# Performance work log

Hardware: AMD Instinct MI355X
Metric: run time of the kernel (lower is better)

The kernel has to match this reference:

```python
import jax, jax.numpy as jnp
import numpy as np

B, N = 16, 4096          # batch, path tokens
D, H = 512, 2048         # dim, 4*dim
NG, NP, NF = 4, 4, 2     # expert counts
GIN, PIN, NC = 4096, 1024, 4
EPS = 1e-5


def _ln_norm(x):
    # LayerNorm normalization (biased var, eps=1e-5), affine applied by caller
    m = jnp.mean(x, axis=-1, keepdims=True)
    v = jnp.var(x, axis=-1, keepdims=True)
    return (x - m) * jax.lax.rsqrt(v + EPS)


def _expert_mlp(xn, ln_g, ln_b, W1, b1, W2, b2):
    # xn: [B,D] or [E,B,D] (pre-normalized); per-expert affine + MLP (GELU exact)
    h = xn * ln_g[:, None, :] + ln_b[:, None, :]            # [E,B,D]
    h = jax.nn.gelu(jnp.einsum('ebd,edh->ebh', h, W1) + b1[:, None, :], approximate=False)
    return jnp.einsum('ebh,ehd->ebd', h, W2) + b2[:, None, :]


def setup_inputs() -> dict:
    key = jax.random.key(0)
    ks = iter(jax.random.split(key, 64))
    nrm = lambda shape, s=0.02: jax.random.normal(next(ks), shape, jnp.float32) * s
    return {
        'F_gene': jax.random.normal(next(ks), (B, GIN), jnp.float32),
        'F_path': jax.random.normal(next(ks), (B, N, PIN), jnp.float32),
        'gene_ln_g': jnp.ones((GIN,)), 'gene_ln_b': jnp.zeros((GIN,)),
        'gene_W': nrm((GIN, D)), 'gene_b': jnp.zeros((D,)),
        'path_ln_g': jnp.ones((PIN,)), 'path_ln_b': jnp.zeros((PIN,)),
        'path_W': nrm((PIN, D)), 'path_b': jnp.zeros((D,)),
        'g_ln_g': jnp.ones((NG, D)), 'g_ln_b': jnp.zeros((NG, D)),
        'g_W1': nrm((NG, D, H)), 'g_b1': jnp.zeros((NG, H)),
        'g_W2': nrm((NG, H, D)), 'g_b2': jnp.zeros((NG, D)),
        'p_q': jax.random.normal(next(ks), (NP, D), jnp.float32),
        'p_ln_g': jnp.ones((NP, D)), 'p_ln_b': jnp.zeros((NP, D)),
        'p_W1': nrm((NP, D, H)), 'p_b1': jnp.zeros((NP, H)),
        'p_W2': nrm((NP, H, D)), 'p_b2': jnp.zeros((NP, D)),
        'f_ln_g': jnp.ones((NF, D)), 'f_ln_b': jnp.zeros((NF, D)),
        'f_W1': nrm((NF, D, H)), 'f_b1': jnp.zeros((NF, H)),
        'f_W2': nrm((NF, H, D)), 'f_b2': jnp.zeros((NF, D)),
        'gg_ln_g': jnp.ones((D,)), 'gg_ln_b': jnp.zeros((D,)),
        'gg_W': nrm((D, NG)), 'gg_b': jnp.zeros((NG,)),
        'pg_ln_g': jnp.ones((D,)), 'pg_ln_b': jnp.zeros((D,)),
        'pg_W': nrm((D, NP)), 'pg_b': jnp.zeros((NP,)),
        'fg_ln_g': jnp.ones((2 * D,)), 'fg_ln_b': jnp.zeros((2 * D,)),
        'fg_W': nrm((2 * D, NF)), 'fg_b': jnp.zeros((NF,)),
        'fin_ln_g': jnp.ones((2 * D,)), 'fin_ln_b': jnp.zeros((2 * D,)),
        'fin_W': nrm((2 * D, D)), 'fin_b': jnp.zeros((D,)),
        'cls_W': nrm((D, NC)), 'cls_b': jnp.zeros((NC,)),
    }


def _forward(F_gene, F_path, gene_ln_g, gene_ln_b, gene_W, gene_b,
             path_ln_g, path_ln_b, path_W, path_b,
             g_ln_g, g_ln_b, g_W1, g_b1, g_W2, g_b2,
             p_q, p_ln_g, p_ln_b, p_W1, p_b1, p_W2, p_b2,
             f_ln_g, f_ln_b, f_W1, f_b1, f_W2, f_b2,
             gg_ln_g, gg_ln_b, gg_W, gg_b,
             pg_ln_g, pg_ln_b, pg_W, pg_b,
             fg_ln_g, fg_ln_b, fg_W, fg_b,
             fin_ln_g, fin_ln_b, fin_W, fin_b, cls_W, cls_b):
    # input projections
    Xg = (_ln_norm(F_gene) * gene_ln_g + gene_ln_b) @ gene_W + gene_b      # [B,D]
    Xp = (_ln_norm(F_path) * path_ln_g + path_ln_b) @ path_W + path_b      # [B,N,D]

    # gene experts: shared gated mixture of MLPs
    wg = jax.nn.softmax((_ln_norm(Xg) * gg_ln_g + gg_ln_b) @ gg_W + gg_b, axis=-1)  # [B,NG]
    g_stack = _expert_mlp(_ln_norm(Xg), g_ln_g, g_ln_b, g_W1, g_b1, g_W2, g_b2)     # [NG,B,D]
    FGIMF = jnp.einsum('be,ebd->bd', wg, g_stack)

    # path experts: per-expert attention pooling over N tokens, then MLP
    Xp_mean = jnp.mean(Xp, axis=1)                                                  # [B,D]
    wp = jax.nn.softmax((_ln_norm(Xp_mean) * pg_ln_g + pg_ln_b) @ pg_W + pg_b, axis=-1)
    attn = jax.nn.softmax(jnp.einsum('bnd,ed->ebn', Xp, p_q), axis=-1)              # [NP,B,N]
    pooled = jnp.einsum('ebn,bnd->ebd', attn, Xp)                                   # [NP,B,D]
    p_stack = _expert_mlp(_ln_norm(pooled), p_ln_g, p_ln_b, p_W1, p_b1, p_W2, p_b2)
    FPIMF = jnp.einsum('be,ebd->bd', wp, p_stack)

    # fusion experts
    fused = jnp.concatenate([FGIMF, FPIMF], axis=-1)                                # [B,2D]
    wf = jax.nn.softmax((_ln_norm(fused) * fg_ln_g + fg_ln_b) @ fg_W + fg_b, axis=-1)
    fused_in = (_ln_norm(fused) * fin_ln_g + fin_ln_b) @ fin_W + fin_b              # [B,D]
    f_stack = _expert_mlp(_ln_norm(fused_in), f_ln_g, f_ln_b, f_W1, f_b1, f_W2, f_b2)
    FIMMF = jnp.einsum('be,ebd->bd', wf, f_stack)

    logits = FIMMF @ cls_W + cls_b
    hazards = jax.nn.sigmoid(logits)
    S = jnp.cumprod(1.0 - hazards, axis=1)
    return hazards, S


def reference(F_gene, F_path, gene_ln_g, gene_ln_b, gene_W, gene_b,
              path_ln_g, path_ln_b, path_W, path_b,
              g_ln_g, g_ln_b, g_W1, g_b1, g_W2, g_b2,
              p_q, p_ln_g, p_ln_b, p_W1, p_b1, p_W2, p_b2,
              f_ln_g, f_ln_b, f_W1, f_b1, f_W2, f_b2,
              gg_ln_g, gg_ln_b, gg_W, gg_b,
              pg_ln_g, pg_ln_b, pg_W, pg_b,
              fg_ln_g, fg_ln_b, fg_W, fg_b,
              fin_ln_g, fin_ln_b, fin_W, fin_b, cls_W, cls_b):
    return _forward(F_gene, F_path, gene_ln_g, gene_ln_b, gene_W, gene_b,
                    path_ln_g, path_ln_b, path_W, path_b,
                    g_ln_g, g_ln_b, g_W1, g_b1, g_W2, g_b2,
                    p_q, p_ln_g, p_ln_b, p_W1, p_b1, p_W2, p_b2,
                    f_ln_g, f_ln_b, f_W1, f_b1, f_W2, f_b2,
                    gg_ln_g, gg_ln_b, gg_W, gg_b,
                    pg_ln_g, pg_ln_b, pg_W, pg_b,
                    fg_ln_g, fg_ln_b, fg_W, fg_b,
                    fin_ln_g, fin_ln_b, fin_W, fin_b, cls_W, cls_b)
```

## Files before the change

### kernel.cpp

```cpp
#include <hip/hip_runtime.h>
#include <math.h>

#define BB 16
#define NTOK 4096
#define DIM 512
#define HID 2048
#define NGE 4
#define NPE 4
#define NFE 2
#define GIN 4096
#define PIN 1024
#define NCLS 4
#define EPS 1e-5f

#define WS_SUMXN   0
#define WS_Z       16384
#define WS_XG      81920
#define WS_FG      90112
#define WS_FP      98304
#define WS_FIMMF   106496
#define WS_POOLED  114688
#define WS_XPMEAN  147456
#define WS_FIN     155648
#define WS_HG      163840
#define WS_HP      294912
#define WS_HF      425984
#define ZERO_TOT   491520
#define WS_MEAN    491520
#define WS_RSTD    557056
#define WS_S       622592
#define WS_QPROJ   884736
#define WS_GMEAN   888832
#define WS_GRSTD   888848
#define WS_WG      888864
#define WS_WP      888928
#define WS_WF      888992
#define WS_UG      889024
#define WS_UP      921792
#define WS_UF      954560
#define WS_TL      970944
#define WS_END     987328

__device__ __forceinline__ float wsum(float v) {
#pragma unroll
    for (int o = 32; o > 0; o >>= 1) v += __shfl_xor(v, o);
    return v;
}
__device__ __forceinline__ float wmax(float v) {
#pragma unroll
    for (int o = 32; o > 0; o >>= 1) v = fmaxf(v, __shfl_xor(v, o));
    return v;
}
__device__ __forceinline__ float gelu_exact(float x) {
    return 0.5f * x * (1.0f + erff(x * 0.70710678118654752f));
}

__global__ __launch_bounds__(256) void k0_init(const float* __restrict__ F_gene,
                                               const float* __restrict__ path_W,
                                               const float* __restrict__ p_q,
                                               const float* __restrict__ path_ln_g,
                                               float* __restrict__ ws) {
    int blk = blockIdx.x, t = threadIdx.x;
    if (blk < 480) {
        ((float4*)ws)[blk * 256 + t] = make_float4(0.f, 0.f, 0.f, 0.f);
    } else if (blk < 496) {
        __shared__ __align__(16) float pq[NPE * DIM];
        for (int i = t; i < NPE * DIM; i += 256) pq[i] = p_q[i];
        __syncthreads();
        int w = t >> 6, lane = t & 63;
        const float4* pq4 = (const float4*)pq;
        for (int i = 0; i < 16; i++) {
            int k = (blk - 480) * 64 + w * 16 + i;
            const float4* wp4 = (const float4*)(path_W + (size_t)k * DIM);
            float4 x0 = wp4[lane], x1 = wp4[lane + 64];
            float sc[NPE];
#pragma unroll
            for (int e = 0; e < NPE; e++) {
                float4 q0 = pq4[e * 128 + lane], q1 = pq4[e * 128 + lane + 64];
                float d = x0.x * q0.x + x0.y * q0.y + x0.z * q0.z + x0.w * q0.w +
                          x1.x * q1.x + x1.y * q1.y + x1.z * q1.z + x1.w * q1.w;
                sc[e] = wsum(d);
            }
            if (lane == 0) {
                float g = path_ln_g[k];
#pragma unroll
                for (int e = 0; e < NPE; e++) ws[WS_QPROJ + e * PIN + k] = g * sc[e];
            }
        }
    } else {
        int b = blk - 496;
        const float4* row = (const float4*)(F_gene + (size_t)b * GIN);
        float s1 = 0.f, s2 = 0.f;
        for (int i = t; i < GIN / 4; i += 256) {
            float4 v = row[i];
            s1 += v.x + v.y + v.z + v.w;
            s2 += v.x * v.x + v.y * v.y + v.z * v.z + v.w * v.w;
        }
        __shared__ float sc[8];
        s1 = wsum(s1); s2 = wsum(s2);
        int w = t >> 6;
        if ((t & 63) == 0) { sc[w] = s1; sc[4 + w] = s2; }
        __syncthreads();
        if (t == 0) {
            float S1 = sc[0] + sc[1] + sc[2] + sc[3];
            float S2 = sc[4] + sc[5] + sc[6] + sc[7];
            float m = S1 / GIN;
            float var = S2 / GIN - m * m;
            ws[WS_GMEAN + b] = m;
            ws[WS_GRSTD + b] = rsqrtf(var + EPS);
        }
    }
}

__global__ __launch_bounds__(256) void k1_pass1(const float* __restrict__ F_path,
                                                float* __restrict__ ws) {
    __shared__ __align__(16) float qlds[NPE * PIN];
    __shared__ __align__(16) float comb[4 * PIN];
    int t = threadIdx.x;
    for (int i = t; i < NPE * PIN; i += 256) qlds[i] = ws[WS_QPROJ + i];
    __syncthreads();
    int blk = blockIdx.x;
    int b = blk >> 6, chunk = blk & 63;
    int w = t >> 6, lane = t & 63;
    const float4* qp4 = (const float4*)qlds;
    float4 sxn[4];
#pragma unroll
    for (int j = 0; j < 4; j++) sxn[j] = make_float4(0.f, 0.f, 0.f, 0.f);
    for (int i = 0; i < 16; i++) {
        int n = chunk * 64 + w * 16 + i;
        const float4* rowp = (const float4*)(F_path + ((size_t)(b * NTOK + n)) * PIN);
        float4 x[4];
#pragma unroll
        for (int j = 0; j < 4; j++) x[j] = rowp[lane + 64 * j];
        float s1 = 0.f, s2 = 0.f;
#pragma unroll
        for (int j = 0; j < 4; j++) {
            s1 += x[j].x + x[j].y + x[j].z + x[j].w;
            s2 += x[j].x * x[j].x + x[j].y * x[j].y + x[j].z * x[j].z + x[j].w * x[j].w;
        }
        s1 = wsum(s1); s2 = wsum(s2);
        float m = s1 * (1.f / PIN);
        float var = s2 * (1.f / PIN) - m * m;
        float r = rsqrtf(var + EPS);
        float sc[NPE];
#pragma unroll
        for (int e = 0; e < NPE; e++) {
            float d = 0.f;
#pragma unroll
            for (int j = 0; j < 4; j++) {
                float4 q = qp4[e * (PIN / 4) + lane + 64 * j];
                d += (x[j].x - m) * q.x + (x[j].y - m) * q.y +
                     (x[j].z - m) * q.z + (x[j].w - m) * q.w;
            }
            sc[e] = wsum(d) * r;
        }
#pragma unroll
        for (int j = 0; j < 4; j++) {
            sxn[j].x += (x[j].x - m) * r;
            sxn[j].y += (x[j].y - m) * r;
            sxn[j].z += (x[j].z - m) * r;
            sxn[j].w += (x[j].w - m) * r;
        }
        if (lane == 0) {
            ws[WS_MEAN + b * NTOK + n] = m;
            ws[WS_RSTD + b * NTOK + n] = r;
#pragma unroll
            for (int e = 0; e < NPE; e++) ws[WS_S + (e * BB + b) * NTOK + n] = sc[e];
        }
    }
    float4* comb4 = (float4*)comb;
#pragma unroll
    for (int j = 0; j < 4; j++) comb4[w * (PIN / 4) + lane + 64 * j] = sxn[j];
    __syncthreads();
    {
        float4 a = comb4[t], bq = comb4[256 + t], c = comb4[512 + t], d = comb4[768 + t];
        atomicAdd(ws + WS_SUMXN + b * PIN + 4 * t + 0, a.x + bq.x + c.x + d.x);
        atomicAdd(ws + WS_SUMXN + b * PIN + 4 * t + 1, a.y + bq.y + c.y + d.y);
        atomicAdd(ws + WS_SUMXN + b * PIN + 4 * t + 2, a.z + bq.z + c.z + d.z);
        atomicAdd(ws + WS_SUMXN + b * PIN + 4 * t + 3, a.w + bq.w + c.w + d.w);
    }
}

__global__ __launch_bounds__(256) void k2_softmax(float* __restrict__ ws) {
    int row = blockIdx.x;
    float* s = ws + WS_S + (size_t)row * NTOK;
    int t = threadIdx.x, w = t >> 6, lane = t & 63;
    __shared__ float sc[4];
    float4 v[4];
    float mx = -1e30f;
#pragma unroll
    for (int j = 0; j < 4; j++) {
        v[j] = ((float4*)s)[t + j * 256];
        mx = fmaxf(mx, fmaxf(fmaxf(v[j].x, v[j].y), fmaxf(v[j].z, v[j].w)));
    }
    mx = wmax(mx);
    if (lane == 0) sc[w] = mx;
    __syncthreads();
    mx = fmaxf(fmaxf(sc[0], sc[1]), fmaxf(sc[2], sc[3]));
    __syncthreads();
    float sum = 0.f;
#pragma unroll
    for (int j = 0; j < 4; j++) {
        v[j].x = __expf(v[j].x - mx); v[j].y = __expf(v[j].y - mx);
        v[j].z = __expf(v[j].z - mx); v[j].w = __expf(v[j].w - mx);
        sum += v[j].x + v[j].y + v[j].z + v[j].w;
    }
    sum = wsum(sum);
    if (lane == 0) sc[w] = sum;
    __syncthreads();
    float inv = 1.f / (sc[0] + sc[1] + sc[2] + sc[3]);
#pragma unroll
    for (int j = 0; j < 4; j++) {
        v[j].x *= inv; v[j].y *= inv; v[j].z *= inv; v[j].w *= inv;
        ((float4*)s)[t + j * 256] = v[j];
    }
}

__global__ __launch_bounds__(256) void k3_pass2(const float* __restrict__ F_path,
                                                const float* __restrict__ F_gene,
                                                const float* __restrict__ gene_W,
                                                const float* __restrict__ gene_ln_g,
                                                const float* __restrict__ gene_ln_b,
                                                float* __restrict__ ws) {
    __shared__ __align__(16) float lds[4096];
    int t = threadIdx.x, blk = blockIdx.x;
    if (blk < 1024) {
        int b = blk >> 6, chunk = blk & 63;
        int w = t >> 6, lane = t & 63;
        float4 zacc[NPE][4];
#pragma unroll
        for (int e = 0; e < NPE; e++)
#pragma unroll
            for (int j = 0; j < 4; j++) zacc[e][j] = make_float4(0.f, 0.f, 0.f, 0.f);
        for (int i = 0; i < 16; i++) {
            int n = chunk * 64 + w * 16 + i;
            const float4* rowp = (const float4*)(F_path + ((size_t)(b * NTOK + n)) * PIN);
            float4 x[4];
#pragma unroll
            for (int j = 0; j < 4; j++) x[j] = rowp[lane + 64 * j];
            float m = ws[WS_MEAN + b * NTOK + n];
            float r = ws[WS_RSTD + b * NTOK + n];
            float ar[NPE];
#pragma unroll
            for (int e = 0; e < NPE; e++) ar[e] = ws[WS_S + (e * BB + b) * NTOK + n] * r;
#pragma unroll
            for (int e = 0; e < NPE; e++) {
#pragma unroll
                for (int j = 0; j < 4; j++) {
                    zacc[e][j].x += ar[e] * (x[j].x - m);
                    zacc[e][j].y += ar[e] * (x[j].y - m);
                    zacc[e][j].z += ar[e] * (x[j].z - m);
                    zacc[e][j].w += ar[e] * (x[j].w - m);
                }
            }
        }
        float4* l4 = (float4*)lds;
        for (int e = 0; e < NPE; e++) {
            __syncthreads();
#pragma unroll
            for (int j = 0; j < 4; j++) l4[w * (PIN / 4) + lane + 64 * j] = zacc[e][j];
            __syncthreads();
            float4 a = l4[t], bq = l4[256 + t], c = l4[512 + t], d = l4[768 + t];
            atomicAdd(ws + WS_Z + (e * BB + b) * PIN + 4 * t + 0, a.x + bq.x + c.x + d.x);
            atomicAdd(ws + WS_Z + (e * BB + b) * PIN + 4 * t + 1, a.y + bq.y + c.y + d.y);
            atomicAdd(ws + WS_Z + (e * BB + b) * PIN + 4 * t + 2, a.z + bq.z + c.z + d.z);
            atomicAdd(ws + WS_Z + (e * BB + b) * PIN + 4 * t + 3, a.w + bq.w + c.w + d.w);
        }
    } else {
        int k0 = (blk - 1024) * 256;
        for (int b = 0; b < BB; b++) {
            float x = F_gene[(size_t)b * GIN + k0 + t];
            float m = ws[WS_GMEAN + b], r = ws[WS_GRSTD + b];
            lds[b * 256 + t] = (x - m) * r * gene_ln_g[k0 + t] + gene_ln_b[k0 + t];
        }
        __syncthreads();
        float acc0[BB], acc1[BB];
#pragma unroll
        for (int b = 0; b < BB; b++) { acc0[b] = 0.f; acc1[b] = 0.f; }
        int d0 = t, d1 = t + 256;
#pragma unroll 8
        for (int kk = 0; kk < 256; kk++) {
            float w0 = gene_W[(size_t)(k0 + kk) * DIM + d0];
            float w1 = gene_W[(size_t)(k0 + kk) * DIM + d1];
#pragma unroll
            for (int b = 0; b < BB; b++) {
                float y = lds[b * 256 + kk];
                acc0[b] += y * w0; acc1[b] += y * w1;
            }
        }
        for (int b = 0; b < BB; b++) {
            atomicAdd(ws + WS_XG + b * DIM + d0, acc0[b]);
            atomicAdd(ws + WS_XG + b * DIM + d1, acc1[b]);
        }
    }
}

__global__ __launch_bounds__(256) void k_skinny(const float* __restrict__ A,
                                                const float* __restrict__ W,
                                                float* __restrict__ out,
                                                const float* __restrict__ lng,
                                                const float* __restrict__ lnb,
                                                const float* __restrict__ ws,
                                                int pool) {
    __shared__ __align__(16) float a[16 * 64];
    int blk = blockIdx.x, t = threadIdx.x;
    int rg = blk >> 4, kc = blk & 15;
    for (int i = t; i < 1024; i += 256) {
        int r = rg * 16 + (i >> 6);
        int k = kc * 64 + (i & 63);
        float v;
        if (pool) {
            v = (r < 64) ? ws[WS_Z + (size_t)r * PIN + k]
                         : ws[WS_SUMXN + (size_t)(r - 64) * PIN + k] * (1.f / NTOK);
            v = v * lng[k] + lnb[k];
        } else {
            v = A[(size_t)r * PIN + k];
        }
        a[i] = v;
    }
    __syncthreads();
    float2 acc[16];
#pragma unroll
    for (int r = 0; r < 16; r++) acc[r] = make_float2(0.f, 0.f);
    int d2 = 2 * t;
#pragma unroll 4
    for (int k = 0; k < 64; k++) {
        float2 wv = *(const float2*)&W[(size_t)(kc * 64 + k) * DIM + d2];
#pragma unroll
        for (int r = 0; r < 16; r++) {
            float av = a[r * 64 + k];
            acc[r].x += av * wv.x;
            acc[r].y += av * wv.y;
        }
    }
#pragma unroll
    for (int r = 0; r < 16; r++) {
        int rr = rg * 16 + r;
        atomicAdd(out + (size_t)rr * DIM + d2 + 0, acc[r].x);
        atomicAdd(out + (size_t)rr * DIM + d2 + 1, acc[r].y);
    }
}

__global__ __launch_bounds__(256) void k5_rows(const float* __restrict__ gene_b,
    const float* __restrict__ path_b,
    const float* __restrict__ gg_ln_g, const float* __restrict__ gg_ln_b,
    const float* __restrict__ gg_W, const float* __restrict__ gg_b,
    const float* __restrict__ pg_ln_g, const float* __restrict__ pg_ln_b,
    const float* __restrict__ pg_W, const float* __restrict__ pg_b,
    const float* __restrict__ g_ln_g, const float* __restrict__ g_ln_b,
    const float* __restrict__ p_ln_g, const float* __restrict__ p_ln_b,
    float* __restrict__ ws) {
    int blk = blockIdx.x, t = threadIdx.x;
    __shared__ float sc[8];
    __shared__ float sc2[16];
    int c0 = t, c1 = t + 256;
    int w = t >> 6, lane = t & 63;
    float v0, v1;
    int type, b = 0, r = 0;
    if (blk < 16) {
        type = 0; b = blk;
        v0 = ws[WS_XG + b * DIM + c0] + gene_b[c0];
        v1 = ws[WS_XG + b * DIM + c1] + gene_b[c1];
    } else if (blk < 32) {
        type = 1; b = blk - 16;
        v0 = ws[WS_XPMEAN + b * DIM + c0] + path_b[c0];
        v1 = ws[WS_XPMEAN + b * DIM + c1] + path_b[c1];
    } else {
        type = 2; r = blk - 32;
        v0 = ws[WS_POOLED + r * DIM + c0] + path_b[c0];
        v1 = ws[WS_POOLED + r * DIM + c1] + path_b[c1];
    }
    float s1 = wsum(v0 + v1), s2 = wsum(v0 * v0 + v1 * v1);
    if (lane == 0) { sc[w] = s1; sc[4 + w] = s2; }
    __syncthreads();
    s1 = sc[0] + sc[1] + sc[2] + sc[3];
    s2 = sc[4] + sc[5] + sc[6] + sc[7];
    float m = s1 / DIM, var = s2 / DIM - m * m, rs = rsqrtf(var + EPS);
    float xn0 = (v0 - m) * rs, xn1 = (v1 - m) * rs;
    if (type == 0) {
#pragma unroll
        for (int e = 0; e < NGE; e++) {
            ws[WS_UG + (e * BB + b) * DIM + c0] = xn0 * g_ln_g[e * DIM + c0] + g_ln_b[e * DIM + c0];
            ws[WS_UG + (e * BB + b) * DIM + c1] = xn1 * g_ln_g[e * DIM + c1] + g_ln_b[e * DIM + c1];
        }
        float t0 = xn0 * gg_ln_g[c0] + gg_ln_b[c0];
        float t1 = xn1 * gg_ln_g[c1] + gg_ln_b[c1];
        float l[4];
#pragma unroll
        for (int e = 0; e < 4; e++) l[e] = wsum(t0 * gg_W[c0 * 4 + e] + t1 * gg_W[c1 * 4 + e]);
        if (lane == 0)
#pragma unroll
            for (int e = 0; e < 4; e++) sc2[w * 4 + e] = l[e];
        __syncthreads();
        if (t == 0) {
            float lg[4], mx = -1e30f;
#pragma unroll
            for (int e = 0; e < 4; e++) {
                lg[e] = sc2[e] + sc2[4 + e] + sc2[8 + e] + sc2[12 + e] + gg_b[e];
                mx = fmaxf(mx, lg[e]);
            }
            float sum = 0.f;
#pragma unroll
            for (int e = 0; e < 4; e++) { lg[e] = __expf(lg[e] - mx); sum += lg[e]; }
#pragma unroll
            for (int e = 0; e < 4; e++) ws[WS_WG + b * NGE + e] = lg[e] / sum;
        }
    } else if (type == 1) {
        float t0 = xn0 * pg_ln_g[c0] + pg_ln_b[c0];
        float t1 = xn1 * pg_ln_g[c1] + pg_ln_b[c1];
        float l[4];
#pragma unroll
        for (int e = 0; e < 4; e++) l[e] = wsum(t0 * pg_W[c0 * 4 + e] + t1 * pg_W[c1 * 4 + e]);
        if (lane == 0)
#pragma unroll
            for (int e = 0; e < 4; e++) sc2[w * 4 + e] = l[e];
        __syncthreads();
        if (t == 0) {
            float lg[4], mx = -1e30f;
#pragma unroll
            for (int e = 0; e < 4; e++) {
                lg[e] = sc2[e] + sc2[4 + e] + sc2[8 + e] + sc2[12 + e] + pg_b[e];
                mx = fmaxf(mx, lg[e]);
            }
            float sum = 0.f;
#pragma unroll
            for (int e = 0; e < 4; e++) { lg[e] = __expf(lg[e] - mx); sum += lg[e]; }
#pragma unroll
            for (int e = 0; e < 4; e++) ws[WS_WP + b * NPE + e] = lg[e] / sum;
        }
    } else {
        int e = r >> 4;
        ws[WS_UP + r * DIM + c0] = xn0 * p_ln_g[e * DIM + c0] + p_ln_b[e * DIM + c0];
        ws[WS_UP + r * DIM + c1] = xn1 * p_ln_g[e * DIM + c1] + p_ln_b[e * DIM + c1];
    }
}

__global__ __launch_bounds__(256) void k_mlp1(const float* __restrict__ U0, const float* __restrict__ W10,
                                              float* __restrict__ H0,
                                              const float* __restrict__ U1, const float* __restrict__ W11,
                                              float* __restrict__ H1,
                                              int halfBlk) {
    __shared__ float a[16 * 64];
    int blk = blockIdx.x, t = threadIdx.x;
    const float* U; const float* W1; float* H;
    int lb;
    if (blk < halfBlk) { U = U0; W1 = W10; H = H0; lb = blk; }
    else               { U = U1; W1 = W11; H = H1; lb = blk - halfBlk; }
    int e = lb >> 5, ht = (lb >> 3) & 3, kc = lb & 7;
    const float* Ue = U + (size_t)e * BB * DIM;
    for (int i = t; i < 1024; i += 256) {
        int b = i >> 6, kk = i & 63;
        a[i] = Ue[b * DIM + kc * 64 + kk];
    }
    __syncthreads();
    float2 acc[BB];
#pragma unroll
    for (int b = 0; b < BB; b++) acc[b] = make_float2(0.f, 0.f);
    int h2 = ht * 512 + 2 * t;
#pragma unroll 4
    for (int kk = 0; kk < 64; kk++) {
        float2 wv = *(const float2*)&W1[((size_t)e * DIM + kc * 64 + kk) * HID + h2];
#pragma unroll
        for (int b = 0; b < BB; b++) {
            float av = a[b * 64 + kk];
            acc[b].x += av * wv.x;
            acc[b].y += av * wv.y;
        }
    }
#pragma unroll
    for (int b = 0; b < BB; b++) {
        atomicAdd(H + (size_t)(e * BB + b) * HID + h2 + 0, acc[b].x);
        atomicAdd(H + (size_t)(e * BB + b) * HID + h2 + 1, acc[b].y);
    }
}

__global__ __launch_bounds__(256) void k_gelu(float* __restrict__ H,
                                              const float* __restrict__ b1a,
                                              const float* __restrict__ b1b,
                                              int eSplit) {
    int idx4 = (blockIdx.x * 256 + threadIdx.x) * 4;
    int e = idx4 >> 15;
    int h = idx4 & (HID - 1);
    const float* bp = (e < eSplit) ? (b1a + (size_t)e * HID) : (b1b + (size_t)(e - eSplit) * HID);
    float4 v = *(float4*)&H[idx4];
    float4 bv = *(const float4*)&bp[h];
    v.x = gelu_exact(v.x + bv.x);
    v.y = gelu_exact(v.y + bv.y);
    v.z = gelu_exact(v.z + bv.z);
    v.w = gelu_exact(v.w + bv.w);
    *(float4*)&H[idx4] = v;
}

__global__ __launch_bounds__(256) void k_mlp2(const float* __restrict__ H0, const float* __restrict__ W20,
                                              const float* __restrict__ gate0, int ng0, float* __restrict__ out0,
                                              const float* __restrict__ H1, const float* __restrict__ W21,
                                              const float* __restrict__ gate1, int ng1, float* __restrict__ out1,
                                              int halfBlk) {
    __shared__ float a[16 * 128];
    int blk = blockIdx.x, t = threadIdx.x;
    const float* H; const float* W2; const float* gate; float* outp;
    int ng, lb;
    if (blk < halfBlk) { H = H0; W2 = W20; gate = gate0; ng = ng0; outp = out0; lb = blk; }
    else               { H = H1; W2 = W21; gate = gate1; ng = ng1; outp = out1; lb = blk - halfBlk; }
    int e = lb >> 4, kc = lb & 15;
    for (int i = t; i < 2048; i += 256) {
        int b = i >> 7, kk = i & 127;
        a[i] = H[(size_t)(e * BB + b) * HID + kc * 128 + kk];
    }
    __syncthreads();
    float2 acc[BB];
#pragma unroll
    for (int b = 0; b < BB; b++) acc[b] = make_float2(0.f, 0.f);
    int d2 = 2 * t;
#pragma unroll 4
    for (int kk = 0; kk < 128; kk++) {
        float2 wv = *(const float2*)&W2[((size_t)e * HID + kc * 128 + kk) * DIM + d2];
#pragma unroll
        for (int b = 0; b < BB; b++) {
            float av = a[b * 128 + kk];
            acc[b].x += av * wv.x;
            acc[b].y += av * wv.y;
        }
    }
#pragma unroll
    for (int b = 0; b < BB; b++) {
        float g = gate[b * ng + e];
        atomicAdd(outp + (size_t)b * DIM + d2 + 0, g * acc[b].x);
        atomicAdd(outp + (size_t)b * DIM + d2 + 1, g * acc[b].y);
    }
}

__global__ __launch_bounds__(256) void k8a(const float* __restrict__ fg_ln_g, const float* __restrict__ fg_ln_b,
                                           const float* __restrict__ fg_W, const float* __restrict__ fg_b,
                                           const float* __restrict__ fin_ln_g, const float* __restrict__ fin_ln_b,
                                           const float* __restrict__ g_b2, const float* __restrict__ p_b2,
                                           float* __restrict__ ws) {
    __shared__ float sc[8];
    __shared__ float sc2[8];
    int b = blockIdx.x, t = threadIdx.x;
    int w = t >> 6, lane = t & 63;
    float wg[4], wp[4];
#pragma unroll
    for (int e = 0; e < 4; e++) { wg[e] = ws[WS_WG + b * 4 + e]; wp[e] = ws[WS_WP + b * 4 + e]; }
    float v[4];
    v[0] = ws[WS_FG + b * DIM + t]
         + wg[0] * g_b2[t] + wg[1] * g_b2[DIM + t] + wg[2] * g_b2[2 * DIM + t] + wg[3] * g_b2[3 * DIM + t];
    v[1] = ws[WS_FG + b * DIM + t + 256]
         + wg[0] * g_b2[t + 256] + wg[1] * g_b2[DIM + t + 256] + wg[2] * g_b2[2 * DIM + t + 256] + wg[3] * g_b2[3 * DIM + t + 256];
    v[2] = ws[WS_FP + b * DIM + t]
         + wp[0] * p_b2[t] + wp[1] * p_b2[DIM + t] + wp[2] * p_b2[2 * DIM + t] + wp[3] * p_b2[3 * DIM + t];
    v[3] = ws[WS_FP + b * DIM + t + 256]
         + wp[0] * p_b2[t + 256] + wp[1] * p_b2[DIM + t + 256] + wp[2] * p_b2[2 * DIM + t + 256] + wp[3] * p_b2[3 * DIM + t + 256];
    float s1 = wsum(v[0] + v[1] + v[2] + v[3]);
    float s2 = wsum(v[0] * v[0] + v[1] * v[1] + v[2] * v[2] + v[3] * v[3]);
    if (lane == 0) { sc[w] = s1; sc[4 + w] = s2; }
    __syncthreads();
    s1 = sc[0] + sc[1] + sc[2] + sc[3];
    s2 = sc[4] + sc[5] + sc[6] + sc[7];
    float m = s1 / (2 * DIM), var = s2 / (2 * DIM) - m * m, rs = rsqrtf(var + EPS);
    float l0 = 0.f, l1 = 0.f;
    int cols[4] = {t, t + 256, t + 512, t + 768};
#pragma unroll
    for (int j = 0; j < 4; j++) {
        int c = cols[j];
        float xn = (v[j] - m) * rs;
        float tf = xn * fg_ln_g[c] + fg_ln_b[c];
        l0 += tf * fg_W[c * 2 + 0];
        l1 += tf * fg_W[c * 2 + 1];
        ws[WS_TL + b * 1024 + c] = xn * fin_ln_g[c] + fin_ln_b[c];
    }
    l0 = wsum(l0); l1 = wsum(l1);
    if (lane == 0) { sc2[w] = l0; sc2[4 + w] = l1; }
    __syncthreads();
    if (t == 0) {
        float L0 = sc2[0] + sc2[1] + sc2[2] + sc2[3] + fg_b[0];
        float L1 = sc2[4] + sc2[5] + sc2[6] + sc2[7] + fg_b[1];
        float mx = fmaxf(L0, L1);
        float p0 = __expf(L0 - mx), p1 = __expf(L1 - mx);
        float inv = 1.f / (p0 + p1);
        ws[WS_WF + b * NFE + 0] = p0 * inv;
        ws[WS_WF + b * NFE + 1] = p1 * inv;
    }
}

__global__ __launch_bounds__(256) void k8b(const float* __restrict__ fin_b,
                                           const float* __restrict__ f_ln_g, const float* __restrict__ f_ln_b,
                                           float* __restrict__ ws) {
    __shared__ float sc[8];
    int b = blockIdx.x, t = threadIdx.x;
    int w = t >> 6, lane = t & 63;
    int c0 = t, c1 = t + 256;
    float a0 = ws[WS_FIN + b * DIM + c0] + fin_b[c0];
    float a1 = ws[WS_FIN + b * DIM + c1] + fin_b[c1];
    float s1 = wsum(a0 + a1), s2 = wsum(a0 * a0 + a1 * a1);
    if (lane == 0) { sc[w] = s1; sc[4 + w] = s2; }
    __syncthreads();
    s1 = sc[0] + sc[1] + sc[2] + sc[3];
    s2 = sc[4] + sc[5] + sc[6] + sc[7];
    float m = s1 / DIM, var = s2 / DIM - m * m, rs = rsqrtf(var + EPS);
    float x0 = (a0 - m) * rs, x1 = (a1 - m) * rs;
#pragma unroll
    for (int e = 0; e < NFE; e++) {
        ws[WS_UF + (e * BB + b) * DIM + c0] = x0 * f_ln_g[e * DIM + c0] + f_ln_b[e * DIM + c0];
        ws[WS_UF + (e * BB + b) * DIM + c1] = x1 * f_ln_g[e * DIM + c1] + f_ln_b[e * DIM + c1];
    }
}

__global__ __launch_bounds__(256) void k11_out(const float* __restrict__ cls_W, const float* __restrict__ cls_b,
                                               const float* __restrict__ f_b2,
                                               const float* __restrict__ ws, float* __restrict__ out) {
    __shared__ float4 red[256];
    __shared__ float hz[64];
    int t = threadIdx.x;
    int b = t >> 4, g = t & 15;
    float wf0 = ws[WS_WF + b * 2 + 0], wf1 = ws[WS_WF + b * 2 + 1];
    float4 acc = make_float4(0.f, 0.f, 0.f, 0.f);
#pragma unroll 8
    for (int k = g; k < DIM; k += 16) {
        float x = ws[WS_FIMMF + b * DIM + k] + wf0 * f_b2[k] + wf1 * f_b2[DIM + k];
        float4 wv = *(const float4*)&cls_W[k * 4];
        acc.x += x * wv.x; acc.y += x * wv.y; acc.z += x * wv.z; acc.w += x * wv.w;
    }
    red[t] = acc;
    __syncthreads();
    if (t < 64) {
        int bb = t >> 2, c = t & 3;
        float s = cls_b[c];
#pragma unroll
        for (int j = 0; j < 16; j++) s += ((const float*)&red[bb * 16 + j])[c];
        hz[t] = 1.f / (1.f + __expf(-s));
    }
    __syncthreads();
    if (t < 64) {
        int bb = t >> 2, c = t & 3;
        float S = 1.f;
        for (int j = 0; j <= c; j++) S *= (1.f - hz[bb * 4 + j]);
        out[t] = hz[t];
        out[64 + t] = S;
    }
}

extern "C" void kernel_launch(void* const* d_in, const int* in_sizes, int n_in,
                              void* d_out, int out_size, void* d_ws, size_t ws_size,
                              hipStream_t stream) {
    (void)in_sizes; (void)n_in; (void)out_size; (void)ws_size;
    const float* F_gene    = (const float*)d_in[0];
    const float* F_path    = (const float*)d_in[1];
    const float* gene_ln_g = (const float*)d_in[2];
    const float* gene_ln_b = (const float*)d_in[3];
    const float* gene_W    = (const float*)d_in[4];
    const float* gene_b    = (const float*)d_in[5];
    const float* path_ln_g = (const float*)d_in[6];
    const float* path_ln_b = (const float*)d_in[7];
    const float* path_W    = (const float*)d_in[8];
    const float* path_b    = (const float*)d_in[9];
    const float* g_ln_g    = (const float*)d_in[10];
    const float* g_ln_b    = (const float*)d_in[11];
    const float* g_W1      = (const float*)d_in[12];
    const float* g_b1      = (const float*)d_in[13];
    const float* g_W2      = (const float*)d_in[14];
    const float* g_b2      = (const float*)d_in[15];
    const float* p_q       = (const float*)d_in[16];
    const float* p_ln_g    = (const float*)d_in[17];
    const float* p_ln_b    = (const float*)d_in[18];
    const float* p_W1      = (const float*)d_in[19];
    const float* p_b1      = (const float*)d_in[20];
    const float* p_W2      = (const float*)d_in[21];
    const float* p_b2      = (const float*)d_in[22];
    const float* f_ln_g    = (const float*)d_in[23];
    const float* f_ln_b    = (const float*)d_in[24];
    const float* f_W1      = (const float*)d_in[25];
    const float* f_b1      = (const float*)d_in[26];
    const float* f_W2      = (const float*)d_in[27];
    const float* f_b2      = (const float*)d_in[28];
    const float* gg_ln_g   = (const float*)d_in[29];
    const float* gg_ln_b   = (const float*)d_in[30];
    const float* gg_W      = (const float*)d_in[31];
    const float* gg_b      = (const float*)d_in[32];
    const float* pg_ln_g   = (const float*)d_in[33];
    const float* pg_ln_b   = (const float*)d_in[34];
    const float* pg_W      = (const float*)d_in[35];
    const float* pg_b      = (const float*)d_in[36];
    const float* fg_ln_g   = (const float*)d_in[37];
    const float* fg_ln_b   = (const float*)d_in[38];
    const float* fg_W      = (const float*)d_in[39];
    const float* fg_b      = (const float*)d_in[40];
    const float* fin_ln_g  = (const float*)d_in[41];
    const float* fin_ln_b  = (const float*)d_in[42];
    const float* fin_W     = (const float*)d_in[43];
    const float* fin_b     = (const float*)d_in[44];
    const float* cls_W     = (const float*)d_in[45];
    const float* cls_b     = (const float*)d_in[46];
    float* ws  = (float*)d_ws;
    float* out = (float*)d_out;

    k0_init<<<512, 256, 0, stream>>>(F_gene, path_W, p_q, path_ln_g, ws);
    k1_pass1<<<1024, 256, 0, stream>>>(F_path, ws);
    k2_softmax<<<64, 256, 0, stream>>>(ws);
    k3_pass2<<<1040, 256, 0, stream>>>(F_path, F_gene, gene_W, gene_ln_g, gene_ln_b, ws);
    k_skinny<<<80, 256, 0, stream>>>(nullptr, path_W, ws + WS_POOLED, path_ln_g, path_ln_b, ws, 1);
    k5_rows<<<96, 256, 0, stream>>>(gene_b, path_b, gg_ln_g, gg_ln_b, gg_W, gg_b,
                                    pg_ln_g, pg_ln_b, pg_W, pg_b,
                                    g_ln_g, g_ln_b, p_ln_g, p_ln_b, ws);
    k_mlp1<<<256, 256, 0, stream>>>(ws + WS_UG, g_W1, ws + WS_HG,
                                    ws + WS_UP, p_W1, ws + WS_HP, 128);
    k_gelu<<<256, 256, 0, stream>>>(ws + WS_HG, g_b1, p_b1, 4);
    k_mlp2<<<128, 256, 0, stream>>>(ws + WS_HG, g_W2, ws + WS_WG, NGE, ws + WS_FG,
                                    ws + WS_HP, p_W2, ws + WS_WP, NPE, ws + WS_FP, 64);
    k8a<<<16, 256, 0, stream>>>(fg_ln_g, fg_ln_b, fg_W, fg_b, fin_ln_g, fin_ln_b, g_b2, p_b2, ws);
    k_skinny<<<16, 256, 0, stream>>>(ws + WS_TL, fin_W, ws + WS_FIN, nullptr, nullptr, ws, 0);
    k8b<<<16, 256, 0, stream>>>(fin_b, f_ln_g, f_ln_b, ws);
    k_mlp1<<<64, 256, 0, stream>>>(ws + WS_UF, f_W1, ws + WS_HF,
                                   ws + WS_UF, f_W1, ws + WS_HF, 64);
    k_gelu<<<64, 256, 0, stream>>>(ws + WS_HF, f_b1, f_b1, 2);
    k_mlp2<<<32, 256, 0, stream>>>(ws + WS_HF, f_W2, ws + WS_WF, NFE, ws + WS_FIMMF,
                                   ws + WS_HF, f_W2, ws + WS_WF, NFE, ws + WS_FIMMF, 32);
    k11_out<<<1, 256, 0, stream>>>(cls_W, cls_b, f_b2, ws, out);
}
```

Baseline: 899.6 us.

## Assign one expert per wavefront in path pooling pass instead of all experts per wave

The path pooling kernel previously had each wavefront handle 16 tokens for all four experts, holding 64 float4 accumulators, then reducing across waves through shared memory with barriers. Now each wavefront handles one expert over all 64 tokens of the chunk, so it keeps only four float4 accumulators and atomically adds straight to global memory with no LDS reduction or barriers. This lowers register pressure and removes synchronisation, but every wave now reads all 64 rows of F_path, so the block issues four times as many global loads, which must be absorbed by cache.

Measured after the change: 852.0 us. -5.3%, faster.

```diff
diff --git a/kernel.cpp b/kernel.cpp
--- a/kernel.cpp
+++ b/kernel.cpp
@@ -227,45 +227,42 @@
     if (blk < 1024) {
         int b = blk >> 6, chunk = blk & 63;
         int w = t >> 6, lane = t & 63;
-        float4 zacc[NPE][4];
-#pragma unroll
-        for (int e = 0; e < NPE; e++)
-#pragma unroll
-            for (int j = 0; j < 4; j++) zacc[e][j] = make_float4(0.f, 0.f, 0.f, 0.f);
-        for (int i = 0; i < 16; i++) {
-            int n = chunk * 64 + w * 16 + i;
+        float4 za = make_float4(0.f, 0.f, 0.f, 0.f);
+        float4 zb = make_float4(0.f, 0.f, 0.f, 0.f);
+        float4 zc = make_float4(0.f, 0.f, 0.f, 0.f);
+        float4 zd = make_float4(0.f, 0.f, 0.f, 0.f);
+        const float* mrow = ws + WS_MEAN + (size_t)b * NTOK;
+        const float* rrow = ws + WS_RSTD + (size_t)b * NTOK;
+        const float* srow = ws + WS_S + ((size_t)(w * BB + b)) * NTOK;
+        int n0 = chunk * 64;
+        for (int i = 0; i < 64; i++) {
+            int n = n0 + i;
             const float4* rowp = (const float4*)(F_path + ((size_t)(b * NTOK + n)) * PIN);
-            float4 x[4];
-#pragma unroll
-            for (int j = 0; j < 4; j++) x[j] = rowp[lane + 64 * j];
-            float m = ws[WS_MEAN + b * NTOK + n];
-            float r = ws[WS_RSTD + b * NTOK + n];
-            float ar[NPE];
-#pragma unroll
-            for (int e = 0; e < NPE; e++) ar[e] = ws[WS_S + (e * BB + b) * NTOK + n] * r;
-#pragma unroll
-            for (int e = 0; e < NPE; e++) {
-#pragma unroll
-                for (int j = 0; j < 4; j++) {
-                    zacc[e][j].x += ar[e] * (x[j].x - m);
-                    zacc[e][j].y += ar[e] * (x[j].y - m);
-                    zacc[e][j].z += ar[e] * (x[j].z - m);
-                    zacc[e][j].w += ar[e] * (x[j].w - m);
-                }
-            }
-        }
-        float4* l4 = (float4*)lds;
-        for (int e = 0; e < NPE; e++) {
-            __syncthreads();
-#pragma unroll
-            for (int j = 0; j < 4; j++) l4[w * (PIN / 4) + lane + 64 * j] = zacc[e][j];
-            __syncthreads();
-            float4 a = l4[t], bq = l4[256 + t], c = l4[512 + t], d = l4[768 + t];
-            atomicAdd(ws + WS_Z + (e * BB + b) * PIN + 4 * t + 0, a.x + bq.x + c.x + d.x);
-            atomicAdd(ws + WS_Z + (e * BB + b) * PIN + 4 * t + 1, a.y + bq.y + c.y + d.y);
-            atomicAdd(ws + WS_Z + (e * BB + b) * PIN + 4 * t + 2, a.z + bq.z + c.z + d.z);
-            atomicAdd(ws + WS_Z + (e * BB + b) * PIN + 4 * t + 3, a.w + bq.w + c.w + d.w);
-        }
+            float4 x0 = rowp[lane];
+            float4 x1 = rowp[lane + 64];
+            float4 x2 = rowp[lane + 128];
+            float4 x3 = rowp[lane + 192];
+            float m = mrow[n];
+            float ar = srow[n] * rrow[n];
+            za.x += ar * (x0.x - m); za.y += ar * (x0.y - m);
+            za.z += ar * (x0.z - m); za.w += ar * (x0.w - m);
+            zb.x += ar * (x1.x - m); zb.y += ar * (x1.y - m);
+            zb.z += ar * (x1.z - m); zb.w += ar * (x1.w - m);
+            zc.x += ar * (x2.x - m); zc.y += ar * (x2.y - m);
+            zc.z += ar * (x2.z - m); zc.w += ar * (x2.w - m);
+            zd.x += ar * (x3.x - m); zd.y += ar * (x3.y - m);
+            zd.z += ar * (x3.z - m); zd.w += ar * (x3.w - m);
+        }
+        float* zp = ws + WS_Z + ((size_t)(w * BB + b)) * PIN;
+        int k0 = 4 * lane;
+        atomicAdd(zp + k0 +   0, za.x); atomicAdd(zp + k0 +   1, za.y);
+        atomicAdd(zp + k0 +   2, za.z); atomicAdd(zp + k0 +   3, za.w);
+        atomicAdd(zp + k0 + 256, zb.x); atomicAdd(zp + k0 + 257, zb.y);
+        atomicAdd(zp + k0 + 258, zb.z); atomicAdd(zp + k0 + 259, zb.w);
+        atomicAdd(zp + k0 + 512, zc.x); atomicAdd(zp + k0 + 513, zc.y);
+        atomicAdd(zp + k0 + 514, zc.z); atomicAdd(zp + k0 + 515, zc.w);
+        atomicAdd(zp + k0 + 768, zd.x); atomicAdd(zp + k0 + 769, zd.y);
+        atomicAdd(zp + k0 + 770, zd.z); atomicAdd(zp + k0 + 771, zd.w);
     } else {
         int k0 = (blk - 1024) * 256;
         for (int b = 0; b < BB; b++) {
@@ -288,6 +285,7 @@
                 acc0[b] += y * w0; acc1[b] += y * w1;
             }
         }
+#pragma unroll
         for (int b = 0; b < BB; b++) {
             atomicAdd(ws + WS_XG + b * DIM + d0, acc0[b]);
             atomicAdd(ws + WS_XG + b * DIM + d1, acc1[b]);
```
